# Kernel tuning notes

Hardware: AMD Instinct MI355X
Metric: run time of the kernel (lower is better)

The kernel has to match this reference:

```python
import jax, jax.numpy as jnp
import numpy as np

N_NODES = 50000
N_EDGES = 800000
IN_F, HID, N_CLS = 128, 128, 40


def gcn_conv(x, row, col, ew, W, b, n):
    # PyG GCNConv with add_self_loops=True, normalize=True (gcn_norm):
    # out = D^{-1/2} (A + I) D^{-1/2} (x W) + b, aggregation at target = col.
    h = x @ W                                        # [N, F_out]
    loop = jnp.arange(n)
    row_f = jnp.concatenate([row, loop])             # self-loop weight = 1
    col_f = jnp.concatenate([col, loop])
    ew_f = jnp.concatenate([ew, jnp.ones((n,), dtype=ew.dtype)])
    deg = jax.ops.segment_sum(ew_f, col_f, num_segments=n)
    dinv = jnp.where(deg > 0, jax.lax.rsqrt(deg), 0.0)
    norm = dinv[row_f] * ew_f * dinv[col_f]          # [E+N]
    msg = norm[:, None] * h[row_f]                   # gather + scale
    out = jax.ops.segment_sum(msg, col_f, num_segments=n)  # scatter-add
    return out + b


def setup_inputs() -> dict:
    key = jax.random.key(0)
    ks = jax.random.split(key, 8)
    glorot = lambda k, fi, fo: jax.random.normal(k, (fi, fo), jnp.float32) * np.sqrt(2.0 / (fi + fo))
    return {
        "x": jax.random.normal(ks[0], (N_NODES, IN_F), jnp.float32),
        "edge_weight": jax.random.uniform(ks[1], (N_EDGES,), jnp.float32),
        "W1": glorot(ks[2], IN_F, HID),
        "b1": jnp.zeros((HID,), jnp.float32),
        "W2": glorot(ks[3], HID, HID),
        "b2": jnp.zeros((HID,), jnp.float32),
        "W3": glorot(ks[4], HID, N_CLS),
        "b3": jnp.zeros((N_CLS,), jnp.float32),
        "edge_index": jax.random.randint(ks[5], (2, N_EDGES), 0, N_NODES, jnp.int64),
        "target_mask": jnp.ones((N_NODES,), jnp.bool_),
    }


def reference(x, edge_weight, W1, b1, W2, b2, W3, b3, edge_index, target_mask):
    n = x.shape[0]
    row, col = edge_index[0], edge_index[1]
    h = gcn_conv(x, row, col, edge_weight, W1, b1, n)
    h = jax.nn.relu(h)  # dropout is identity in eval mode
    h = gcn_conv(h, row, col, edge_weight, W2, b2, n)
    h = jax.nn.relu(h)
    h = gcn_conv(h, row, col, edge_weight, W3, b3, n)
    return h[target_mask]
```

## Files before the change

### kernel.cpp

```cpp
#include <hip/hip_runtime.h>
#include <hip/hip_fp16.h>

#define N_NODES 50000
#define N_EDGES 800000
#define IN_F 128
#define HID 128
#define N_CLS 40
#define SCAN_BLOCKS 196
#define GEMM_TILE_ROWS 32
#define GEMM_BLOCKS 1563
#define CNT_BLOCKS 3125
#define DEG_SCALE 2097152.0f
#define DEG_MASK ((1ull << 44) - 1)

static inline int cdiv(int a, int b) { return (a + b - 1) / b; }

__device__ __forceinline__ void count_deg_body(int e, const int* __restrict__ col,
                                               const float* __restrict__ ew,
                                               unsigned long long* __restrict__ packed) {
    if (e < N_EDGES) {
        int c = col[e];
        unsigned long long v =
            (1ull << 44) | (unsigned long long)__float2uint_rn(ew[e] * DEG_SCALE);
        atomicAdd(&packed[c], v);
    }
}

__device__ __forceinline__ void gemm128_body(int b, const float* __restrict__ X,
                                             const float* __restrict__ W,
                                             __half* __restrict__ out) {
    __shared__ float xsT[IN_F][GEMM_TILE_ROWS + 4];
    __shared__ float wch[32][128];
    const int t = threadIdx.x;
    const int row0 = b * GEMM_TILE_ROWS;

    #pragma unroll
    for (int i = 0; i < 4; ++i) {
        int idx = t + i * 256;
        int row = idx >> 5;
        int k4  = idx & 31;
        float4 v = make_float4(0.f, 0.f, 0.f, 0.f);
        if (row0 + row < N_NODES)
            v = *(const float4*)&X[(size_t)(row0 + row) * IN_F + k4 * 4];
        xsT[k4 * 4 + 0][row] = v.x;
        xsT[k4 * 4 + 1][row] = v.y;
        xsT[k4 * 4 + 2][row] = v.z;
        xsT[k4 * 4 + 3][row] = v.w;
    }

    const int c0 = (t & 31) * 4;
    const int r0 = (t >> 5) * 4;
    float acc[4][4];
    #pragma unroll
    for (int i = 0; i < 4; ++i)
        #pragma unroll
        for (int j = 0; j < 4; ++j) acc[i][j] = 0.f;

    for (int kk = 0; kk < IN_F; kk += 32) {
        __syncthreads();
        #pragma unroll
        for (int i = 0; i < 4; ++i) {
            int idx = t + i * 256;
            int wr = idx >> 5;
            int wc4 = idx & 31;
            *(float4*)&wch[wr][wc4 * 4] =
                *(const float4*)&W[(size_t)(kk + wr) * 128 + wc4 * 4];
        }
        __syncthreads();
        #pragma unroll 4
        for (int k = 0; k < 32; ++k) {
            float4 a = *(const float4*)&xsT[kk + k][r0];
            float4 w = *(const float4*)&wch[k][c0];
            acc[0][0] = fmaf(a.x, w.x, acc[0][0]);
            acc[0][1] = fmaf(a.x, w.y, acc[0][1]);
            acc[0][2] = fmaf(a.x, w.z, acc[0][2]);
            acc[0][3] = fmaf(a.x, w.w, acc[0][3]);
            acc[1][0] = fmaf(a.y, w.x, acc[1][0]);
            acc[1][1] = fmaf(a.y, w.y, acc[1][1]);
            acc[1][2] = fmaf(a.y, w.z, acc[1][2]);
            acc[1][3] = fmaf(a.y, w.w, acc[1][3]);
            acc[2][0] = fmaf(a.z, w.x, acc[2][0]);
            acc[2][1] = fmaf(a.z, w.y, acc[2][1]);
            acc[2][2] = fmaf(a.z, w.z, acc[2][2]);
            acc[2][3] = fmaf(a.z, w.w, acc[2][3]);
            acc[3][0] = fmaf(a.w, w.x, acc[3][0]);
            acc[3][1] = fmaf(a.w, w.y, acc[3][1]);
            acc[3][2] = fmaf(a.w, w.z, acc[3][2]);
            acc[3][3] = fmaf(a.w, w.w, acc[3][3]);
        }
    }

    #pragma unroll
    for (int i = 0; i < 4; ++i) {
        int r = row0 + r0 + i;
        if (r < N_NODES) {
            union { __half2 h2[2]; float2 f2; } u;
            u.h2[0] = __floats2half2_rn(acc[i][0], acc[i][1]);
            u.h2[1] = __floats2half2_rn(acc[i][2], acc[i][3]);
            *(float2*)&out[(size_t)r * 128 + c0] = u.f2;
        }
    }
}

__global__ __launch_bounds__(256) void gemm128_kernel(const float* __restrict__ X,
                                                      const float* __restrict__ W,
                                                      __half* __restrict__ out) {
    gemm128_body(blockIdx.x, X, W, out);
}

__global__ __launch_bounds__(256) void fused_gemm1_count(
    const float* __restrict__ X, const float* __restrict__ W, __half* __restrict__ out,
    const int* __restrict__ col, const float* __restrict__ ew,
    unsigned long long* __restrict__ packed) {
    int id = blockIdx.x;
    if (id & 1) {
        count_deg_body((id >> 1) * 256 + threadIdx.x, col, ew, packed);
    } else {
        int b = id >> 1;
        if (b < GEMM_BLOCKS) gemm128_body(b, X, W, out);
    }
}

__global__ void scan_reduce_dinv(const unsigned long long* __restrict__ packed,
                                 int* __restrict__ blockSums, float* __restrict__ dinv) {
    __shared__ int s[256];
    int i = blockIdx.x * 256 + threadIdx.x;
    unsigned long long p = (i < N_NODES) ? packed[i] : 0ull;
    if (i < N_NODES)
        dinv[i] = rsqrtf((float)(p & DEG_MASK) * (1.0f / DEG_SCALE) + 1.0f);
    s[threadIdx.x] = (int)(p >> 44);
    __syncthreads();
    for (int off = 128; off > 0; off >>= 1) {
        if (threadIdx.x < off) s[threadIdx.x] += s[threadIdx.x + off];
        __syncthreads();
    }
    if (threadIdx.x == 0) blockSums[blockIdx.x] = s[0];
}

__global__ void scan_offsets(const int* __restrict__ blockSums, int* __restrict__ offsets) {
    __shared__ int s[256];
    int t = threadIdx.x;
    int v = (t < SCAN_BLOCKS) ? blockSums[t] : 0;
    s[t] = v;
    __syncthreads();
    for (int off = 1; off < 256; off <<= 1) {
        int tmp = (t >= off) ? s[t - off] : 0;
        __syncthreads();
        s[t] += tmp;
        __syncthreads();
    }
    offsets[t] = s[t] - v;
}

__global__ void scan_final(const unsigned long long* __restrict__ packed,
                           const int* __restrict__ offsets,
                           int* __restrict__ row_ptr, int* __restrict__ cursor) {
    __shared__ int s[256];
    int t = threadIdx.x;
    int i = blockIdx.x * 256 + t;
    int v = (i < N_NODES) ? (int)(packed[i] >> 44) : 0;
    s[t] = v;
    __syncthreads();
    for (int off = 1; off < 256; off <<= 1) {
        int tmp = (t >= off) ? s[t - off] : 0;
        __syncthreads();
        s[t] += tmp;
        __syncthreads();
    }
    int incl = s[t] + offsets[blockIdx.x];
    if (i < N_NODES) {
        int excl = incl - v;
        row_ptr[i] = excl;
        cursor[i] = excl;
        if (i == N_NODES - 1) row_ptr[N_NODES] = incl;
    }
}

__global__ void fill_kernel(const int* __restrict__ row, const int* __restrict__ col,
                            const float* __restrict__ ew, const float* __restrict__ dinv,
                            int* __restrict__ cursor, uint2* __restrict__ csr) {
    int e = blockIdx.x * blockDim.x + threadIdx.x;
    if (e >= N_EDGES) return;
    int r = row[e];
    int c = col[e];
    int pos = atomicAdd(&cursor[c], 1);
    float w = dinv[r] * ew[e] * dinv[c];
    csr[pos] = make_uint2((unsigned)r, __float_as_uint(w));
}

__global__ void gemm40_kernel(const float* __restrict__ X, const float* __restrict__ W,
                              __half* __restrict__ out) {
    __shared__ float xs[16 * IN_F];
    const int row0 = blockIdx.x * 16;
    for (int i = threadIdx.x; i < 16 * IN_F; i += 256)
        xs[i] = X[(size_t)row0 * IN_F + i];
    __syncthreads();
    for (int idx = threadIdx.x; idx < 16 * N_CLS; idx += 256) {
        int r = idx / N_CLS;
        int c = idx % N_CLS;
        float acc = 0.f;
        #pragma unroll 8
        for (int k = 0; k < IN_F; ++k)
            acc = fmaf(xs[r * IN_F + k], W[k * N_CLS + c], acc);
        out[(size_t)(row0 + r) * N_CLS + c] = __float2half(acc);
    }
}

__device__ __forceinline__ void fma_h4(float w, uint2 g, float4& acc) {
    float2 lo = __half22float2(*(const __half2*)&g.x);
    float2 hi = __half22float2(*(const __half2*)&g.y);
    acc.x = fmaf(w, lo.x, acc.x);
    acc.y = fmaf(w, lo.y, acc.y);
    acc.z = fmaf(w, hi.x, acc.z);
    acc.w = fmaf(w, hi.y, acc.w);
}

template <bool RELU>
__global__ __launch_bounds__(256) void agg128_kernel(
    const int* __restrict__ row_ptr, const uint2* __restrict__ csr,
    const __half* __restrict__ h, const float* __restrict__ dinv,
    const float* __restrict__ b, float* __restrict__ out) {
    int wave = threadIdx.x >> 6;
    int lane = threadIdx.x & 63;
    int sub  = lane >> 5;
    int sl   = lane & 31;
    int node = blockIdx.x * 8 + wave * 2 + sub;
    if (node >= N_NODES) return;
    int beg = row_ptr[node];
    int end = row_ptr[node + 1];
    int f = sl * 4;
    float4 acc = make_float4(0.f, 0.f, 0.f, 0.f);

    int k = beg;
    for (; k + 4 <= end; k += 4) {
        uint2 e0 = csr[k];
        uint2 e1 = csr[k + 1];
        uint2 e2 = csr[k + 2];
        uint2 e3 = csr[k + 3];
        uint2 g0 = *(const uint2*)&h[(size_t)e0.x * 128 + f];
        uint2 g1 = *(const uint2*)&h[(size_t)e1.x * 128 + f];
        uint2 g2 = *(const uint2*)&h[(size_t)e2.x * 128 + f];
        uint2 g3 = *(const uint2*)&h[(size_t)e3.x * 128 + f];
        fma_h4(__uint_as_float(e0.y), g0, acc);
        fma_h4(__uint_as_float(e1.y), g1, acc);
        fma_h4(__uint_as_float(e2.y), g2, acc);
        fma_h4(__uint_as_float(e3.y), g3, acc);
    }
    for (; k < end; ++k) {
        uint2 e = csr[k];
        uint2 g = *(const uint2*)&h[(size_t)e.x * 128 + f];
        fma_h4(__uint_as_float(e.y), g, acc);
    }

    float di = dinv[node];
    float di2 = di * di;
    uint2 gs = *(const uint2*)&h[(size_t)node * 128 + f];
    fma_h4(di2, gs, acc);
    float4 bb = *(const float4*)&b[f];
    acc.x += bb.x; acc.y += bb.y; acc.z += bb.z; acc.w += bb.w;
    if (RELU) {
        acc.x = fmaxf(acc.x, 0.f);
        acc.y = fmaxf(acc.y, 0.f);
        acc.z = fmaxf(acc.z, 0.f);
        acc.w = fmaxf(acc.w, 0.f);
    }
    *(float4*)&out[(size_t)node * 128 + f] = acc;
}

__global__ __launch_bounds__(256) void agg40_kernel(
    const int* __restrict__ row_ptr, const uint2* __restrict__ csr,
    const __half* __restrict__ h, const float* __restrict__ dinv,
    const float* __restrict__ b, float* __restrict__ out) {
    int wave = threadIdx.x >> 6;
    int lane = threadIdx.x & 63;
    int node = blockIdx.x * 4 + wave;
    if (node >= N_NODES || lane >= N_CLS) return;
    int beg = row_ptr[node];
    int end = row_ptr[node + 1];
    float acc = 0.f;
    int k = beg;
    for (; k + 4 <= end; k += 4) {
        uint2 e0 = csr[k];
        uint2 e1 = csr[k + 1];
        uint2 e2 = csr[k + 2];
        uint2 e3 = csr[k + 3];
        float g0 = __half2float(h[(size_t)e0.x * N_CLS + lane]);
        float g1 = __half2float(h[(size_t)e1.x * N_CLS + lane]);
        float g2 = __half2float(h[(size_t)e2.x * N_CLS + lane]);
        float g3 = __half2float(h[(size_t)e3.x * N_CLS + lane]);
        acc = fmaf(__uint_as_float(e0.y), g0, acc);
        acc = fmaf(__uint_as_float(e1.y), g1, acc);
        acc = fmaf(__uint_as_float(e2.y), g2, acc);
        acc = fmaf(__uint_as_float(e3.y), g3, acc);
    }
    for (; k < end; ++k) {
        uint2 e = csr[k];
        acc = fmaf(__uint_as_float(e.y),
                   __half2float(h[(size_t)e.x * N_CLS + lane]), acc);
    }
    float di = dinv[node];
    acc = fmaf(di * di, __half2float(h[(size_t)node * N_CLS + lane]), acc) + b[lane];
    out[(size_t)node * N_CLS + lane] = acc;
}

extern "C" void kernel_launch(void* const* d_in, const int* in_sizes, int n_in,
                              void* d_out, int out_size, void* d_ws, size_t ws_size,
                              hipStream_t stream) {
    const float* x  = (const float*)d_in[0];
    const float* ew = (const float*)d_in[1];
    const float* W1 = (const float*)d_in[2];
    const float* b1 = (const float*)d_in[3];
    const float* W2 = (const float*)d_in[4];
    const float* b2 = (const float*)d_in[5];
    const float* W3 = (const float*)d_in[6];
    const float* b3 = (const float*)d_in[7];
    const int*   ei = (const int*)d_in[8];
    const int* row = ei;
    const int* col = ei + N_EDGES;
    float* out = (float*)d_out;

    char* ws = (char*)d_ws;
    size_t off = 0;
    auto alloc = [&](size_t bytes) -> void* {
        void* p = (void*)(ws + off);
        off = (off + bytes + 255) & ~(size_t)255;
        return p;
    };
    unsigned long long* packed = (unsigned long long*)alloc((size_t)N_NODES * 8);
    float*  dinv      = (float*)alloc((size_t)N_NODES * 4);
    int*    blockSums = (int*)alloc(256 * 4);
    int*    offsets   = (int*)alloc(256 * 4);
    int*    row_ptr   = (int*)alloc((size_t)(N_NODES + 1) * 4);
    int*    cursor    = (int*)alloc((size_t)N_NODES * 4);
    uint2*  csr       = (uint2*)alloc((size_t)N_EDGES * 8);
    __half* h16       = (__half*)alloc((size_t)N_NODES * HID * 2);
    float*  hagg      = (float*)alloc((size_t)N_NODES * HID * 4);

    hipMemsetAsync(packed, 0, (size_t)N_NODES * 8, stream);

    fused_gemm1_count<<<2 * CNT_BLOCKS, 256, 0, stream>>>(x, W1, h16, col, ew, packed);

    scan_reduce_dinv<<<SCAN_BLOCKS, 256, 0, stream>>>(packed, blockSums, dinv);
    scan_offsets<<<1, 256, 0, stream>>>(blockSums, offsets);
    scan_final<<<SCAN_BLOCKS, 256, 0, stream>>>(packed, offsets, row_ptr, cursor);
    fill_kernel<<<cdiv(N_EDGES, 256), 256, 0, stream>>>(row, col, ew, dinv, cursor, csr);

    const int agg128_blocks = cdiv(N_NODES, 8);
    const int agg40_blocks  = cdiv(N_NODES, 4);

    agg128_kernel<true><<<agg128_blocks, 256, 0, stream>>>(row_ptr, csr, h16, dinv, b1, hagg);

    gemm128_kernel<<<GEMM_BLOCKS, 256, 0, stream>>>(hagg, W2, h16);
    agg128_kernel<true><<<agg128_blocks, 256, 0, stream>>>(row_ptr, csr, h16, dinv, b2, hagg);

    gemm40_kernel<<<N_NODES / 16, 256, 0, stream>>>(hagg, W3, h16);
    agg40_kernel<<<agg40_blocks, 256, 0, stream>>>(row_ptr, csr, h16, dinv, b3, out);
}
```

Before: 360.5 us.

## Fuse aggregation with next-layer GEMM and replace three-pass scan with lookback

Each 128-wide aggregation now writes its 32-row tile straight into shared memory, and the following GEMM (W2 or W3) consumes it there. This removes the fp32 hagg round trip through global memory and two kernel launches. The three-kernel prefix scan becomes a single decoupled-lookback scan that uses a zeroed state array, and the aggregation inner loop is unrolled to 8 edges. The cost is fewer blocks (one per 32 rows) doing serial gather work, which may hurt latency hiding, plus spin-waiting in the scan that relies on blocks being scheduled forward.

After: 469.3 us. 1.3x slower.

```diff
diff --git a/kernel.cpp b/kernel.cpp
--- a/kernel.cpp
+++ b/kernel.cpp
@@ -3,17 +3,17 @@
 
 #define N_NODES 50000
 #define N_EDGES 800000
-#define IN_F 128
 #define HID 128
 #define N_CLS 40
-#define SCAN_BLOCKS 196
-#define GEMM_TILE_ROWS 32
-#define GEMM_BLOCKS 1563
+#define SCAN_CHUNKS 196
+#define TILES32 1563
 #define CNT_BLOCKS 3125
 #define DEG_SCALE 2097152.0f
 #define DEG_MASK ((1ull << 44) - 1)
 
 static inline int cdiv(int a, int b) { return (a + b - 1) / b; }
+
+struct GemmSmem { float xsT[128][36]; float wch[16][128]; };
 
 __device__ __forceinline__ void count_deg_body(int e, const int* __restrict__ col,
                                                const float* __restrict__ ew,
@@ -26,28 +26,28 @@
     }
 }
 
-__device__ __forceinline__ void gemm128_body(int b, const float* __restrict__ X,
+template <bool SKIP_STAGE>
+__device__ __forceinline__ void gemm128_tile(int tile, const float* __restrict__ X,
                                              const float* __restrict__ W,
-                                             __half* __restrict__ out) {
-    __shared__ float xsT[IN_F][GEMM_TILE_ROWS + 4];
-    __shared__ float wch[32][128];
+                                             __half* __restrict__ out, GemmSmem& s) {
     const int t = threadIdx.x;
-    const int row0 = b * GEMM_TILE_ROWS;
-
-    #pragma unroll
-    for (int i = 0; i < 4; ++i) {
-        int idx = t + i * 256;
-        int row = idx >> 5;
-        int k4  = idx & 31;
-        float4 v = make_float4(0.f, 0.f, 0.f, 0.f);
-        if (row0 + row < N_NODES)
-            v = *(const float4*)&X[(size_t)(row0 + row) * IN_F + k4 * 4];
-        xsT[k4 * 4 + 0][row] = v.x;
-        xsT[k4 * 4 + 1][row] = v.y;
-        xsT[k4 * 4 + 2][row] = v.z;
-        xsT[k4 * 4 + 3][row] = v.w;
-    }
-
+    const int row0 = tile * 32;
+    if (!SKIP_STAGE) {
+        __syncthreads();
+        #pragma unroll
+        for (int i = 0; i < 4; ++i) {
+            int idx = t + i * 256;
+            int row = idx >> 5;
+            int k4  = idx & 31;
+            float4 v = make_float4(0.f, 0.f, 0.f, 0.f);
+            if (row0 + row < N_NODES)
+                v = *(const float4*)&X[(size_t)(row0 + row) * 128 + k4 * 4];
+            s.xsT[k4 * 4 + 0][row] = v.x;
+            s.xsT[k4 * 4 + 1][row] = v.y;
+            s.xsT[k4 * 4 + 2][row] = v.z;
+            s.xsT[k4 * 4 + 3][row] = v.w;
+        }
+    }
     const int c0 = (t & 31) * 4;
     const int r0 = (t >> 5) * 4;
     float acc[4][4];
@@ -56,21 +56,21 @@
         #pragma unroll
         for (int j = 0; j < 4; ++j) acc[i][j] = 0.f;
 
-    for (int kk = 0; kk < IN_F; kk += 32) {
+    for (int kk = 0; kk < 128; kk += 16) {
         __syncthreads();
         #pragma unroll
-        for (int i = 0; i < 4; ++i) {
+        for (int i = 0; i < 2; ++i) {
             int idx = t + i * 256;
             int wr = idx >> 5;
             int wc4 = idx & 31;
-            *(float4*)&wch[wr][wc4 * 4] =
+            *(float4*)&s.wch[wr][wc4 * 4] =
                 *(const float4*)&W[(size_t)(kk + wr) * 128 + wc4 * 4];
         }
         __syncthreads();
         #pragma unroll 4
-        for (int k = 0; k < 32; ++k) {
-            float4 a = *(const float4*)&xsT[kk + k][r0];
-            float4 w = *(const float4*)&wch[k][c0];
+        for (int k = 0; k < 16; ++k) {
+            float4 a = *(const float4*)&s.xsT[kk + k][r0];
+            float4 w = *(const float4*)&s.wch[k][c0];
             acc[0][0] = fmaf(a.x, w.x, acc[0][0]);
             acc[0][1] = fmaf(a.x, w.y, acc[0][1]);
             acc[0][2] = fmaf(a.x, w.z, acc[0][2]);
@@ -89,7 +89,6 @@
             acc[3][3] = fmaf(a.w, w.w, acc[3][3]);
         }
     }
-
     #pragma unroll
     for (int i = 0; i < 4; ++i) {
         int r = row0 + r0 + i;
@@ -102,45 +101,32 @@
     }
 }
 
-__global__ __launch_bounds__(256) void gemm128_kernel(const float* __restrict__ X,
-                                                      const float* __restrict__ W,
-                                                      __half* __restrict__ out) {
-    gemm128_body(blockIdx.x, X, W, out);
-}
-
 __global__ __launch_bounds__(256) void fused_gemm1_count(
     const float* __restrict__ X, const float* __restrict__ W, __half* __restrict__ out,
     const int* __restrict__ col, const float* __restrict__ ew,
     unsigned long long* __restrict__ packed) {
+    __shared__ GemmSmem sm;
     int id = blockIdx.x;
     if (id & 1) {
         count_deg_body((id >> 1) * 256 + threadIdx.x, col, ew, packed);
     } else {
         int b = id >> 1;
-        if (b < GEMM_BLOCKS) gemm128_body(b, X, W, out);
-    }
-}
-
-__global__ void scan_reduce_dinv(const unsigned long long* __restrict__ packed,
-                                 int* __restrict__ blockSums, float* __restrict__ dinv) {
+        if (b < TILES32) gemm128_tile<false>(b, X, W, out, sm);
+    }
+}
+
+__global__ __launch_bounds__(256) void scan_lookback(
+    const unsigned long long* __restrict__ packed, unsigned long long* __restrict__ state,
+    float* __restrict__ dinv, int* __restrict__ row_ptr, int* __restrict__ cursor) {
     __shared__ int s[256];
-    int i = blockIdx.x * 256 + threadIdx.x;
+    __shared__ int s_run;
+    const int t = threadIdx.x;
+    const int b = blockIdx.x;
+    const int i = b * 256 + t;
     unsigned long long p = (i < N_NODES) ? packed[i] : 0ull;
     if (i < N_NODES)
         dinv[i] = rsqrtf((float)(p & DEG_MASK) * (1.0f / DEG_SCALE) + 1.0f);
-    s[threadIdx.x] = (int)(p >> 44);
-    __syncthreads();
-    for (int off = 128; off > 0; off >>= 1) {
-        if (threadIdx.x < off) s[threadIdx.x] += s[threadIdx.x + off];
-        __syncthreads();
-    }
-    if (threadIdx.x == 0) blockSums[blockIdx.x] = s[0];
-}
-
-__global__ void scan_offsets(const int* __restrict__ blockSums, int* __restrict__ offsets) {
-    __shared__ int s[256];
-    int t = threadIdx.x;
-    int v = (t < SCAN_BLOCKS) ? blockSums[t] : 0;
+    int v = (int)(p >> 44);
     s[t] = v;
     __syncthreads();
     for (int off = 1; off < 256; off <<= 1) {
@@ -149,30 +135,38 @@
         s[t] += tmp;
         __syncthreads();
     }
-    offsets[t] = s[t] - v;
-}
-
-__global__ void scan_final(const unsigned long long* __restrict__ packed,
-                           const int* __restrict__ offsets,
-                           int* __restrict__ row_ptr, int* __restrict__ cursor) {
-    __shared__ int s[256];
-    int t = threadIdx.x;
-    int i = blockIdx.x * 256 + t;
-    int v = (i < N_NODES) ? (int)(packed[i] >> 44) : 0;
-    s[t] = v;
+    if (t == 0) {
+        int Sb = s[255];
+        if (b == 0) {
+            __hip_atomic_store(&state[0], (2ull << 32) | (unsigned)Sb,
+                               __ATOMIC_RELAXED, __HIP_MEMORY_SCOPE_AGENT);
+            s_run = 0;
+        } else {
+            __hip_atomic_store(&state[b], (1ull << 32) | (unsigned)Sb,
+                               __ATOMIC_RELAXED, __HIP_MEMORY_SCOPE_AGENT);
+            unsigned run = 0;
+            int j = b - 1;
+            while (j >= 0) {
+                unsigned long long st = __hip_atomic_load(&state[j], __ATOMIC_RELAXED,
+                                                          __HIP_MEMORY_SCOPE_AGENT);
+                unsigned flag = (unsigned)(st >> 32);
+                if (flag == 0) { __builtin_amdgcn_s_sleep(1); continue; }
+                run += (unsigned)st;
+                if (flag == 2u) break;
+                --j;
+            }
+            __hip_atomic_store(&state[b], (2ull << 32) | (unsigned)(run + (unsigned)Sb),
+                               __ATOMIC_RELAXED, __HIP_MEMORY_SCOPE_AGENT);
+            s_run = (int)run;
+        }
+    }
     __syncthreads();
-    for (int off = 1; off < 256; off <<= 1) {
-        int tmp = (t >= off) ? s[t - off] : 0;
-        __syncthreads();
-        s[t] += tmp;
-        __syncthreads();
-    }
-    int incl = s[t] + offsets[blockIdx.x];
+    int run = s_run;
     if (i < N_NODES) {
-        int excl = incl - v;
+        int excl = run + s[t] - v;
         row_ptr[i] = excl;
         cursor[i] = excl;
-        if (i == N_NODES - 1) row_ptr[N_NODES] = incl;
+        if (i == N_NODES - 1) row_ptr[N_NODES] = excl + v;
     }
 }
 
@@ -188,24 +182,6 @@
     csr[pos] = make_uint2((unsigned)r, __float_as_uint(w));
 }
 
-__global__ void gemm40_kernel(const float* __restrict__ X, const float* __restrict__ W,
-                              __half* __restrict__ out) {
-    __shared__ float xs[16 * IN_F];
-    const int row0 = blockIdx.x * 16;
-    for (int i = threadIdx.x; i < 16 * IN_F; i += 256)
-        xs[i] = X[(size_t)row0 * IN_F + i];
-    __syncthreads();
-    for (int idx = threadIdx.x; idx < 16 * N_CLS; idx += 256) {
-        int r = idx / N_CLS;
-        int c = idx % N_CLS;
-        float acc = 0.f;
-        #pragma unroll 8
-        for (int k = 0; k < IN_F; ++k)
-            acc = fmaf(xs[r * IN_F + k], W[k * N_CLS + c], acc);
-        out[(size_t)(row0 + r) * N_CLS + c] = __float2half(acc);
-    }
-}
-
 __device__ __forceinline__ void fma_h4(float w, uint2 g, float4& acc) {
     float2 lo = __half22float2(*(const __half2*)&g.x);
     float2 hi = __half22float2(*(const __half2*)&g.y);
@@ -215,28 +191,39 @@
     acc.w = fmaf(w, hi.y, acc.w);
 }
 
-template <bool RELU>
-__global__ __launch_bounds__(256) void agg128_kernel(
-    const int* __restrict__ row_ptr, const uint2* __restrict__ csr,
-    const __half* __restrict__ h, const float* __restrict__ dinv,
-    const float* __restrict__ b, float* __restrict__ out) {
-    int wave = threadIdx.x >> 6;
-    int lane = threadIdx.x & 63;
-    int sub  = lane >> 5;
-    int sl   = lane & 31;
-    int node = blockIdx.x * 8 + wave * 2 + sub;
-    if (node >= N_NODES) return;
+__device__ __forceinline__ float4 agg128_node(int node, int sl,
+                                              const int* __restrict__ row_ptr,
+                                              const uint2* __restrict__ csr,
+                                              const __half* __restrict__ h,
+                                              const float* __restrict__ dinv,
+                                              const float* __restrict__ b) {
     int beg = row_ptr[node];
     int end = row_ptr[node + 1];
     int f = sl * 4;
     float4 acc = make_float4(0.f, 0.f, 0.f, 0.f);
-
     int k = beg;
+    for (; k + 8 <= end; k += 8) {
+        uint2 e0 = csr[k], e1 = csr[k+1], e2 = csr[k+2], e3 = csr[k+3];
+        uint2 e4 = csr[k+4], e5 = csr[k+5], e6 = csr[k+6], e7 = csr[k+7];
+        uint2 g0 = *(const uint2*)&h[(size_t)e0.x * 128 + f];
+        uint2 g1 = *(const uint2*)&h[(size_t)e1.x * 128 + f];
+        uint2 g2 = *(const uint2*)&h[(size_t)e2.x * 128 + f];
+        uint2 g3 = *(const uint2*)&h[(size_t)e3.x * 128 + f];
+        uint2 g4 = *(const uint2*)&h[(size_t)e4.x * 128 + f];
+        uint2 g5 = *(const uint2*)&h[(size_t)e5.x * 128 + f];
+        uint2 g6 = *(const uint2*)&h[(size_t)e6.x * 128 + f];
+        uint2 g7 = *(const uint2*)&h[(size_t)e7.x * 128 + f];
+        fma_h4(__uint_as_float(e0.y), g0, acc);
+        fma_h4(__uint_as_float(e1.y), g1, acc);
+        fma_h4(__uint_as_float(e2.y), g2, acc);
+        fma_h4(__uint_as_float(e3.y), g3, acc);
+        fma_h4(__uint_as_float(e4.y), g4, acc);
+        fma_h4(__uint_as_float(e5.y), g5, acc);
+        fma_h4(__uint_as_float(e6.y), g6, acc);
+        fma_h4(__uint_as_float(e7.y), g7, acc);
+    }
     for (; k + 4 <= end; k += 4) {
-        uint2 e0 = csr[k];
-        uint2 e1 = csr[k + 1];
-        uint2 e2 = csr[k + 2];
-        uint2 e3 = csr[k + 3];
+        uint2 e0 = csr[k], e1 = csr[k+1], e2 = csr[k+2], e3 = csr[k+3];
         uint2 g0 = *(const uint2*)&h[(size_t)e0.x * 128 + f];
         uint2 g1 = *(const uint2*)&h[(size_t)e1.x * 128 + f];
         uint2 g2 = *(const uint2*)&h[(size_t)e2.x * 128 + f];
@@ -251,20 +238,72 @@
         uint2 g = *(const uint2*)&h[(size_t)e.x * 128 + f];
         fma_h4(__uint_as_float(e.y), g, acc);
     }
-
     float di = dinv[node];
-    float di2 = di * di;
     uint2 gs = *(const uint2*)&h[(size_t)node * 128 + f];
-    fma_h4(di2, gs, acc);
+    fma_h4(di * di, gs, acc);
     float4 bb = *(const float4*)&b[f];
-    acc.x += bb.x; acc.y += bb.y; acc.z += bb.z; acc.w += bb.w;
-    if (RELU) {
-        acc.x = fmaxf(acc.x, 0.f);
-        acc.y = fmaxf(acc.y, 0.f);
-        acc.z = fmaxf(acc.z, 0.f);
-        acc.w = fmaxf(acc.w, 0.f);
-    }
-    *(float4*)&out[(size_t)node * 128 + f] = acc;
+    acc.x = fmaxf(acc.x + bb.x, 0.f);
+    acc.y = fmaxf(acc.y + bb.y, 0.f);
+    acc.z = fmaxf(acc.z + bb.z, 0.f);
+    acc.w = fmaxf(acc.w + bb.w, 0.f);
+    return acc;
+}
+
+__device__ __forceinline__ void agg_tile_to_lds(int row0, const int* row_ptr,
+                                                const uint2* csr, const __half* h,
+                                                const float* dinv, const float* bias,
+                                                float (*xsT)[36]) {
+    int wave = threadIdx.x >> 6;
+    int lane = threadIdx.x & 63;
+    int sub  = lane >> 5;
+    int sl   = lane & 31;
+    int f = sl * 4;
+    #pragma unroll
+    for (int i = 0; i < 4; ++i) {
+        int r = i * 8 + wave * 2 + sub;
+        int node = row0 + r;
+        float4 acc = make_float4(0.f, 0.f, 0.f, 0.f);
+        if (node < N_NODES)
+            acc = agg128_node(node, sl, row_ptr, csr, h, dinv, bias);
+        xsT[f + 0][r] = acc.x;
+        xsT[f + 1][r] = acc.y;
+        xsT[f + 2][r] = acc.z;
+        xsT[f + 3][r] = acc.w;
+    }
+}
+
+__global__ __launch_bounds__(256) void agg_gemm128_kernel(
+    const int* __restrict__ row_ptr, const uint2* __restrict__ csr,
+    const __half* __restrict__ h, const float* __restrict__ dinv,
+    const float* __restrict__ bias, const float* __restrict__ W,
+    __half* __restrict__ out) {
+    __shared__ GemmSmem sm;
+    const int row0 = blockIdx.x * 32;
+    agg_tile_to_lds(row0, row_ptr, csr, h, dinv, bias, sm.xsT);
+    __syncthreads();
+    gemm128_tile<true>(blockIdx.x, nullptr, W, out, sm);
+}
+
+__global__ __launch_bounds__(256) void agg_gemm40_kernel(
+    const int* __restrict__ row_ptr, const uint2* __restrict__ csr,
+    const __half* __restrict__ h, const float* __restrict__ dinv,
+    const float* __restrict__ bias, const float* __restrict__ W3,
+    __half* __restrict__ out) {
+    __shared__ float xsT[128][36];
+    const int row0 = blockIdx.x * 32;
+    agg_tile_to_lds(row0, row_ptr, csr, h, dinv, bias, xsT);
+    __syncthreads();
+    for (int idx = threadIdx.x; idx < 32 * N_CLS; idx += 256) {
+        int r = idx / N_CLS;
+        int c = idx % N_CLS;
+        float acc = 0.f;
+        #pragma unroll 8
+        for (int k = 0; k < 128; ++k)
+            acc = fmaf(xsT[k][r], W3[k * N_CLS + c], acc);
+        int node = row0 + r;
+        if (node < N_NODES)
+            out[(size_t)node * N_CLS + c] = __float2half(acc);
+    }
 }
 
 __global__ __launch_bounds__(256) void agg40_kernel(
@@ -280,10 +319,7 @@
     float acc = 0.f;
     int k = beg;
     for (; k + 4 <= end; k += 4) {
-        uint2 e0 = csr[k];
-        uint2 e1 = csr[k + 1];
-        uint2 e2 = csr[k + 2];
-        uint2 e3 = csr[k + 3];
+        uint2 e0 = csr[k], e1 = csr[k+1], e2 = csr[k+2], e3 = csr[k+3];
         float g0 = __half2float(h[(size_t)e0.x * N_CLS + lane]);
         float g1 = __half2float(h[(size_t)e1.x * N_CLS + lane]);
         float g2 = __half2float(h[(size_t)e2.x * N_CLS + lane]);
@@ -326,33 +362,23 @@
         off = (off + bytes + 255) & ~(size_t)255;
         return p;
     };
+    unsigned long long* state  = (unsigned long long*)alloc((size_t)SCAN_CHUNKS * 8);
     unsigned long long* packed = (unsigned long long*)alloc((size_t)N_NODES * 8);
-    float*  dinv      = (float*)alloc((size_t)N_NODES * 4);
-    int*    blockSums = (int*)alloc(256 * 4);
-    int*    offsets   = (int*)alloc(256 * 4);
-    int*    row_ptr   = (int*)alloc((size_t)(N_NODES + 1) * 4);
-    int*    cursor    = (int*)alloc((size_t)N_NODES * 4);
-    uint2*  csr       = (uint2*)alloc((size_t)N_EDGES * 8);
-    __half* h16       = (__half*)alloc((size_t)N_NODES * HID * 2);
-    float*  hagg      = (float*)alloc((size_t)N_NODES * HID * 4);
-
-    hipMemsetAsync(packed, 0, (size_t)N_NODES * 8, stream);
-
-    fused_gemm1_count<<<2 * CNT_BLOCKS, 256, 0, stream>>>(x, W1, h16, col, ew, packed);
-
-    scan_reduce_dinv<<<SCAN_BLOCKS, 256, 0, stream>>>(packed, blockSums, dinv);
-    scan_offsets<<<1, 256, 0, stream>>>(blockSums, offsets);
-    scan_final<<<SCAN_BLOCKS, 256, 0, stream>>>(packed, offsets, row_ptr, cursor);
-    fill_kernel<<<cdiv(N_EDGES, 256), 256, 0, stream>>>(row, col, ew, dinv, cursor, csr);
-
-    const int agg128_blocks = cdiv(N_NODES, 8);
-    const int agg40_blocks  = cdiv(N_NODES, 4);
-
-    agg128_kernel<true><<<agg128_blocks, 256, 0, stream>>>(row_ptr, csr, h16, dinv, b1, hagg);
-
-    gemm128_kernel<<<GEMM_BLOCKS, 256, 0, stream>>>(hagg, W2, h16);
-    agg128_kernel<true><<<agg128_blocks, 256, 0, stream>>>(row_ptr, csr, h16, dinv, b2, hagg);
-
-    gemm40_kernel<<<N_NODES / 16, 256, 0, stream>>>(hagg, W3, h16);
-    agg40_kernel<<<agg40_blocks, 256, 0, stream>>>(row_ptr, csr, h16, dinv, b3, out);
-}
+    size_t zero_bytes = (size_t)((char*)packed - (char*)state) + (size_t)N_NODES * 8;
+    float*  dinv    = (float*)alloc((size_t)N_NODES * 4);
+    int*    row_ptr = (int*)alloc((size_t)(N_NODES + 1) * 4);
+    int*    cursor  = (int*)alloc((size_t)N_NODES * 4);
+    uint2*  csr     = (uint2*)alloc((size_t)N_EDGES * 8);
+    __half* h16a    = (__half*)alloc((size_t)N_NODES * HID * 2);
+    __half* h16b    = (__half*)alloc((size_t)N_NODES * HID * 2);
+    __half* h40     = (__half*)alloc((size_t)N_NODES * N_CLS * 2);
+
+    hipMemsetAsync(state, 0, zero_bytes, stream);
+
+    fused_gemm1_count<<<2 * CNT_BLOCKS, 256, 0, stream>>>(x, W1, h16a, col, ew, packed);
+    scan_lookback<<<SCAN_CHUNKS, 256, 0, stream>>>(packed, state, dinv, row_ptr, cursor);
+    fill_kernel<<<CNT_BLOCKS, 256, 0, stream>>>(row, col, ew, dinv, cursor, csr);
+    agg_gemm128_kernel<<<TILES32, 256, 0, stream>>>(row_ptr, csr, h16a, dinv, b1, W2, h16b);
+    agg_gemm40_kernel<<<TILES32, 256, 0, stream>>>(row_ptr, csr, h16b, dinv, b2, W3, h40);
+    agg40_kernel<<<cdiv(N_NODES, 4), 256, 0, stream>>>(row_ptr, csr, h40, dinv, b3, out);
+}
```
